# Optimization experiments

Hardware: AMD Instinct MI355X
Metric: run time of the kernel (lower is better)

## Reference

```python
import jax, jax.numpy as jnp
import numpy as np

N = 50000      # nodes
E = 1600000    # edges
IN = 128       # in_dim
HID = 128      # hidden_dim
H = 8          # heads
C = HID // H   # out_channels per head
ED = 32        # edge_feat_dim
EPS = 1e-5


def layer_norm(x, g, b):
    mu = x.mean(-1, keepdims=True)
    var = ((x - mu) ** 2).mean(-1, keepdims=True)
    return (x - mu) * jax.lax.rsqrt(var + EPS) * g + b


def setup_inputs() -> dict:
    key = jax.random.key(0)
    ks = jax.random.split(key, 24)
    w = lambda k, s, sc=0.05: (jax.random.normal(k, s, jnp.float32) * sc)
    return dict(
        x=jax.random.normal(ks[0], (N, IN), jnp.float32),
        edge_index=jax.random.randint(ks[1], (2, E), 0, N),
        edge_feats=jax.random.normal(ks[2], (E, ED), jnp.float32),
        # TransformerConv params
        Wq=w(ks[3], (IN, HID)), bq=jnp.zeros((HID,), jnp.float32),
        Wk=w(ks[4], (IN, HID)), bk=jnp.zeros((HID,), jnp.float32),
        Wv=w(ks[5], (IN, HID)), bv=jnp.zeros((HID,), jnp.float32),
        We=w(ks[6], (ED, HID)), be=jnp.zeros((HID,), jnp.float32),
        Wskip=w(ks[7], (IN, HID)), bskip=jnp.zeros((HID,), jnp.float32),
        Wbeta=w(ks[8], (3 * HID, 1)),
        ln1_g=jnp.ones((HID,), jnp.float32), ln1_b=jnp.zeros((HID,), jnp.float32),
        # GlobalContextLayer params
        Wr=w(ks[9], (HID, HID)), br=jnp.zeros((HID,), jnp.float32),
        Ww=w(ks[10], (HID, HID)), bw=jnp.zeros((HID,), jnp.float32),
        Wg=w(ks[11], (2 * HID, HID)), bg=jnp.zeros((HID,), jnp.float32),
        ln2_g=jnp.ones((HID,), jnp.float32), ln2_b=jnp.zeros((HID,), jnp.float32),
    )


def reference(x, edge_index, edge_feats,
              Wq, bq, Wk, bk, Wv, bv, We, be, Wskip, bskip, Wbeta,
              ln1_g, ln1_b, Wr, br, Ww, bw, Wg, bg, ln2_g, ln2_b):
    src, dst = edge_index[0], edge_index[1]  # messages flow src -> dst
    q = (x @ Wq + bq).reshape(N, H, C)
    k = (x @ Wk + bk).reshape(N, H, C)
    v = (x @ Wv + bv).reshape(N, H, C)
    e = (edge_feats @ We + be).reshape(E, H, C)

    k_e = k[src] + e                                   # [E,H,C]
    alpha = (q[dst] * k_e).sum(-1) / jnp.sqrt(jnp.float32(C))  # [E,H]
    # segment softmax over incoming edges of each dst node
    m = jax.ops.segment_max(alpha, dst, num_segments=N)        # [N,H]
    ex = jnp.exp(alpha - m[dst])
    s = jax.ops.segment_sum(ex, dst, num_segments=N)
    alpha = ex / (s[dst] + 1e-16)                      # [E,H]

    msg = (v[src] + e) * alpha[..., None]              # [E,H,C]
    out = jax.ops.segment_sum(msg, dst, num_segments=N).reshape(N, HID)

    # beta skip connection
    x_r = x @ Wskip + bskip
    beta = jax.nn.sigmoid(jnp.concatenate([out, x_r, out - x_r], -1) @ Wbeta)  # [N,1]
    out = beta * x_r + (1.0 - beta) * out

    # block: relu(LN(dropout(out) + residual)); dropout=0, residual_proj=None
    h = jax.nn.relu(layer_norm(out + x, ln1_g, ln1_b))

    # GlobalContextLayer
    g = jax.nn.relu(h.mean(0) @ Wr + br)               # [HID]
    g_bc = g @ Ww + bw                                 # [HID], broadcast to all nodes
    gate = jax.nn.sigmoid(jnp.concatenate([h, jnp.broadcast_to(g_bc, h.shape)], -1) @ Wg + bg)
    return layer_norm(h + gate * g_bc, ln2_g, ln2_b)
```

## Files before the change

kernel.cpp:

```cpp
#include <hip/hip_runtime.h>
#include <hip/hip_fp16.h>

#define NN 50000
#define EE 1600000
#define NB_HIST 1024
#define NB_PROJ 1563
#define NB_SCAN 49

typedef float f4v __attribute__((ext_vector_type(4)));

static __device__ __forceinline__ float4 f4z() { return make_float4(0.f, 0.f, 0.f, 0.f); }


__global__ __launch_bounds__(1024) void scan1_kernel(const int* __restrict__ counts,
                                                     int* __restrict__ offsets,
                                                     int* __restrict__ bsum)
{
    __shared__ int wsum[16];
    __shared__ int wpre[16];
    const int t = threadIdx.x;
    const int lane = t & 63, wid = t >> 6;
    const int i = blockIdx.x * 1024 + t;
    int orig = (i < NN) ? counts[i] : 0;
    int val = orig;
    #pragma unroll
    for (int ofs = 1; ofs < 64; ofs <<= 1) {
        int n = __shfl_up(val, ofs);
        if (lane >= ofs) val += n;
    }
    if (lane == 63) wsum[wid] = val;
    __syncthreads();
    if (t < 16) {
        int w = wsum[t];
        #pragma unroll
        for (int ofs = 1; ofs < 16; ofs <<= 1) {
            int n = __shfl_up(w, ofs);
            if (t >= ofs) w += n;
        }
        wpre[t] = w;
    }
    __syncthreads();
    int incl = val + (wid ? wpre[wid - 1] : 0);
    if (i < NN) offsets[i] = incl - orig;
    if (t == 1023) bsum[blockIdx.x] = incl;
}

__global__ __launch_bounds__(64) void scan2_kernel(int* __restrict__ bsum,
                                                   int* __restrict__ bpre)
{
    const int t = threadIdx.x;
    int orig = (t < NB_SCAN) ? bsum[t] : 0;
    int val = orig;
    #pragma unroll
    for (int ofs = 1; ofs < 64; ofs <<= 1) {
        int n = __shfl_up(val, ofs);
        if (t >= ofs) val += n;
    }
    if (t < NB_SCAN) bpre[t] = val - orig;
}

__global__ __launch_bounds__(1024) void scan3_kernel(int* __restrict__ offsets,
                                                     int* __restrict__ cursor,
                                                     const int* __restrict__ bpre)
{
    const int i = blockIdx.x * 1024 + threadIdx.x;
    const int add = bpre[blockIdx.x];
    if (i < NN) {
        int off = offsets[i] + add;
        offsets[i] = off;
        cursor[i] = off;
    } else if (i == NN) {
        offsets[NN] = EE;
    }
}


__global__ __launch_bounds__(256) void scatter_kernel(const int* __restrict__ ei,
                                                      int* __restrict__ cursor,
                                                      int2* __restrict__ sorted2)
{
    int i = blockIdx.x * blockDim.x + threadIdx.x;
    int stride = gridDim.x * blockDim.x;
    for (; i < EE; i += stride) {
        int srcn = ei[i];
        int d = ei[EE + i];
        int pos = atomicAdd(&cursor[d], 1);
        sorted2[pos] = make_int2(i, srcn);
    }
    if (blockIdx.x == 0 && threadIdx.x < 32) sorted2[EE + threadIdx.x] = make_int2(0, 0);
}


__global__ __launch_bounds__(256) void k1_kernel(
    const int* __restrict__ ei, int* __restrict__ counts,
    const float* __restrict__ x,
    const float* __restrict__ Wq, const float* __restrict__ bq,
    const float* __restrict__ Wk, const float* __restrict__ bk,
    const float* __restrict__ Wv, const float* __restrict__ bv,
    const float* __restrict__ Ws, const float* __restrict__ bs,
    const float* __restrict__ We,
    float* __restrict__ q, __half2* __restrict__ kvh,
    float* __restrict__ xr, __half* __restrict__ qeh)
{
    const int tid = threadIdx.x;
    if (blockIdx.x < NB_HIST) {
        int i = blockIdx.x * 256 + tid;
        int stride = NB_HIST * 256;
        for (; i < EE; i += stride) atomicAdd(&counts[ei[EE + i]], 1);
        return;
    }
    __shared__ float xs[32][132];
    __shared__ float WeS[32 * 129];
    const int row0 = (blockIdx.x - NB_HIST) * 32;
    for (int i = tid; i < 4096; i += 256) WeS[(i >> 7) * 129 + (i & 127)] = We[i];
    for (int i = tid; i < 1024; i += 256) {
        int r = i >> 5, c4 = i & 31;
        int gr = row0 + r;
        float4 val = f4z();
        if (gr < NN) val = ((const float4*)(x + (size_t)gr * 128))[c4];
        ((float4*)xs[r])[c4] = val;
    }
    __syncthreads();
    const int cg = tid & 31;
    const int rg = tid >> 5;
    float4 aq[4], ak[4], av[4], as_[4];
    #pragma unroll
    for (int r = 0; r < 4; ++r) { aq[r] = f4z(); ak[r] = f4z(); av[r] = f4z(); as_[r] = f4z(); }
    #pragma unroll 2
    for (int kk = 0; kk < 128; ++kk) {
        float4 wq = ((const float4*)(Wq + kk * 128))[cg];
        float4 wk = ((const float4*)(Wk + kk * 128))[cg];
        float4 wv = ((const float4*)(Wv + kk * 128))[cg];
        float4 ws = ((const float4*)(Ws + kk * 128))[cg];
        #pragma unroll
        for (int r = 0; r < 4; ++r) {
            float xv = xs[4 * rg + r][kk];
            aq[r].x += xv * wq.x; aq[r].y += xv * wq.y; aq[r].z += xv * wq.z; aq[r].w += xv * wq.w;
            ak[r].x += xv * wk.x; ak[r].y += xv * wk.y; ak[r].z += xv * wk.z; ak[r].w += xv * wk.w;
            av[r].x += xv * wv.x; av[r].y += xv * wv.y; av[r].z += xv * wv.z; av[r].w += xv * wv.w;
            as_[r].x += xv * ws.x; as_[r].y += xv * ws.y; as_[r].z += xv * ws.z; as_[r].w += xv * ws.w;
        }
    }
    const float4 bq4 = ((const float4*)bq)[cg];
    const float4 bk4 = ((const float4*)bk)[cg];
    const float4 bv4 = ((const float4*)bv)[cg];
    const float4 bs4 = ((const float4*)bs)[cg];
    __syncthreads();
    #pragma unroll
    for (int r = 0; r < 4; ++r) {
        int gr = row0 + 4 * rg + r;
        if (gr >= NN) continue;
        float4 o;
        o.x = aq[r].x + bq4.x; o.y = aq[r].y + bq4.y; o.z = aq[r].z + bq4.z; o.w = aq[r].w + bq4.w;
        ((float4*)(q + (size_t)gr * 128))[cg] = o;
        ((float4*)xs[4 * rg + r])[cg] = o;
        float kx = ak[r].x + bk4.x, ky = ak[r].y + bk4.y, kz = ak[r].z + bk4.z, kw = ak[r].w + bk4.w;
        float vx = av[r].x + bv4.x, vy = av[r].y + bv4.y, vz = av[r].z + bv4.z, vw = av[r].w + bv4.w;
        union { __half2 h2[4]; float4 f4; } up;
        up.h2[0] = __floats2half2_rn(kx, vx);
        up.h2[1] = __floats2half2_rn(ky, vy);
        up.h2[2] = __floats2half2_rn(kz, vz);
        up.h2[3] = __floats2half2_rn(kw, vw);
        *((float4*)(kvh + (size_t)gr * 128 + 4 * cg)) = up.f4;
        o.x = as_[r].x + bs4.x; o.y = as_[r].y + bs4.y; o.z = as_[r].z + bs4.z; o.w = as_[r].w + bs4.w;
        ((float4*)(xr + (size_t)gr * 128))[cg] = o;
    }
    __syncthreads();
    const int row = tid >> 3;
    const int j = tid & 7;
    const int gr2 = row0 + row;
    if (gr2 < NN) {
        const float* xrow = xs[row];
        #pragma unroll
        for (int hh = 0; hh < 8; ++hh) {
            float a0 = 0.f, a1 = 0.f, a2 = 0.f, a3 = 0.f;
            #pragma unroll
            for (int c = 0; c < 16; ++c) {
                float qv = xrow[hh * 16 + c];
                const float* wb = &WeS[(j * 4) * 129 + hh * 16 + c];
                a0 += qv * wb[0];
                a1 += qv * wb[129];
                a2 += qv * wb[258];
                a3 += qv * wb[387];
            }
            union { __half2 h2[2]; unsigned long long u64; } u;
            u.h2[0] = __floats2half2_rn(a0, a1);
            u.h2[1] = __floats2half2_rn(a2, a3);
            *(unsigned long long*)(qeh + (size_t)gr2 * 256 + hh * 32 + j * 4) = u.u64;
        }
    }
}


__global__ __launch_bounds__(256) void attn_kernel(
    const float* __restrict__ efeat,
    const float* __restrict__ We, const float* __restrict__ be,
    const float* __restrict__ q, const __half* __restrict__ qeh,
    const __half2* __restrict__ kvh,
    const float* __restrict__ xr, const float* __restrict__ x,
    const float* __restrict__ Wbeta,
    const float* __restrict__ ln1g, const float* __restrict__ ln1b,
    const int* __restrict__ offsets, const int2* __restrict__ sorted2,
    float* __restrict__ h, float* __restrict__ colsum)
{
    __shared__ float WeS[32][128];
    __shared__ float cs[4][128];
    const int tid = threadIdx.x;
    for (int i = tid; i < 4096; i += 256) ((float*)WeS)[i] = We[i];
    const int lane = tid & 63;
    const int wid = tid >> 6;
    const int f0 = 2 * lane;
    const int l8 = lane & 7;
    const int grp = lane & 56;

    const float be0 = be[f0], be1 = be[f0 + 1];
    const float wbo0 = Wbeta[f0],       wbo1 = Wbeta[f0 + 1];
    const float wbr0 = Wbeta[128 + f0], wbr1 = Wbeta[128 + f0 + 1];
    const float wbd0 = Wbeta[256 + f0], wbd1 = Wbeta[256 + f0 + 1];
    const float lg0 = ln1g[f0], lg1 = ln1g[f0 + 1];
    const float lb0 = ln1b[f0], lb1 = ln1b[f0 + 1];

    cs[wid][f0] = 0.f; cs[wid][f0 + 1] = 0.f;
    __syncthreads();

    const int gwave = blockIdx.x * 4 + wid;
    const int nwave = gridDim.x * 4;

    for (int node = gwave; node < NN; node += nwave) {
        const int beg = offsets[node];
        const int end = offsets[node + 1];
        const float2 qv = *(const float2*)(q + (size_t)node * 128 + f0);
        union { float2 f2; __half2 h2[2]; } uq;
        uq.f2 = *(const float2*)(qeh + (size_t)node * 256 + 4 * lane);
        const float2 qe01 = __half22float2(uq.h2[0]);
        const float2 qe23 = __half22float2(uq.h2[1]);
        const float4 qev = make_float4(qe01.x, qe01.y, qe23.x, qe23.y);
        float qbe = qv.x * be0 + qv.y * be1;
        qbe += __shfl_xor(qbe, 1); qbe += __shfl_xor(qbe, 2); qbe += __shfl_xor(qbe, 4);
        const float qbe25 = qbe * 0.25f;

        float m = -1e30f, s = 0.f, a0 = 0.f, a1 = 0.f;
        float4 wef = f4z();

        if (beg < end) {
            int2 esA[8], esB[8];
            f4v efA[8], efB[8];
            float2 kvA[8], kvB[8];

            #pragma unroll
            for (int u = 0; u < 8; ++u) esA[u] = sorted2[beg + u];
            #pragma unroll
            for (int u = 0; u < 8; ++u) {
                efA[u] = __builtin_nontemporal_load(
                    (const f4v*)(efeat + (size_t)esA[u].x * 32 + 4 * l8));
                kvA[u] = *(const float2*)(kvh + (size_t)esA[u].y * 128 + f0);
            }
            #pragma unroll
            for (int u = 0; u < 8; ++u) esB[u] = sorted2[beg + 8 + u];

            auto phase = [&](f4v (&efC)[8], float2 (&kvC)[8],
                             f4v (&efN)[8], float2 (&kvN)[8],
                             int2 (&idxN)[8], int2 (&idxF)[8], int t) {
                #pragma unroll
                for (int u = 0; u < 8; ++u) {
                    efN[u] = __builtin_nontemporal_load(
                        (const f4v*)(efeat + (size_t)idxN[u].x * 32 + 4 * l8));
                    kvN[u] = *(const float2*)(kvh + (size_t)idxN[u].y * 128 + f0);
                }
                #pragma unroll
                for (int u = 0; u < 8; ++u) idxF[u] = sorted2[t + 16 + u];

                const int cnt = end - t;
                float lgt[8]; float2 vfl[8];
                #pragma unroll
                for (int u = 0; u < 8; ++u) {
                    union { float2 f2; __half2 h2[2]; } uk; uk.f2 = kvC[u];
                    float2 k0v0 = __half22float2(uk.h2[0]);
                    float2 k1v1 = __half22float2(uk.h2[1]);
                    vfl[u] = make_float2(k0v0.y, k1v1.y);
                    float part = qv.x * k0v0.x + qv.y * k1v1.x
                               + qev.x * efC[u][0] + qev.y * efC[u][1]
                               + qev.z * efC[u][2] + qev.w * efC[u][3];
                    part += __shfl_xor(part, 1);
                    part += __shfl_xor(part, 2);
                    part += __shfl_xor(part, 4);
                    lgt[u] = (u < cnt) ? (part * 0.25f + qbe25) : -1e30f;
                }
                float m01 = fmaxf(lgt[0], lgt[1]), m23 = fmaxf(lgt[2], lgt[3]);
                float m45 = fmaxf(lgt[4], lgt[5]), m67 = fmaxf(lgt[6], lgt[7]);
                float bm = fmaxf(fmaxf(m01, m23), fmaxf(m45, m67));
                float p[8];
                #pragma unroll
                for (int u = 0; u < 8; ++u) p[u] = __expf(lgt[u] - bm);
                float bsA = 0.f, bsB = 0.f, b0A = 0.f, b0B = 0.f, b1A = 0.f, b1B = 0.f;
                float4 befA = f4z(), befB = f4z();
                #pragma unroll
                for (int u = 0; u < 8; u += 2) {
                    bsA += p[u];     bsB += p[u + 1];
                    b0A = fmaf(p[u], vfl[u].x, b0A);        b0B = fmaf(p[u + 1], vfl[u + 1].x, b0B);
                    b1A = fmaf(p[u], vfl[u].y, b1A);        b1B = fmaf(p[u + 1], vfl[u + 1].y, b1B);
                    befA.x = fmaf(p[u], efC[u][0], befA.x); befB.x = fmaf(p[u + 1], efC[u + 1][0], befB.x);
                    befA.y = fmaf(p[u], efC[u][1], befA.y); befB.y = fmaf(p[u + 1], efC[u + 1][1], befB.y);
                    befA.z = fmaf(p[u], efC[u][2], befA.z); befB.z = fmaf(p[u + 1], efC[u + 1][2], befB.z);
                    befA.w = fmaf(p[u], efC[u][3], befA.w); befB.w = fmaf(p[u + 1], efC[u + 1][3], befB.w);
                }
                const float nm = fmaxf(m, bm);
                const float so = __expf(m - nm);
                const float sn = __expf(bm - nm);
                s  = s  * so + (bsA + bsB) * sn;
                a0 = a0 * so + (b0A + b0B) * sn;
                a1 = a1 * so + (b1A + b1B) * sn;
                wef.x = wef.x * so + (befA.x + befB.x) * sn;
                wef.y = wef.y * so + (befA.y + befB.y) * sn;
                wef.z = wef.z * so + (befA.z + befB.z) * sn;
                wef.w = wef.w * so + (befA.w + befB.w) * sn;
                m = nm;
            };

            int t = beg;
            while (true) {
                phase(efA, kvA, efB, kvB, esB, esA, t); t += 8; if (t >= end) break;
                phase(efB, kvB, efA, kvA, esA, esB, t); t += 8; if (t >= end) break;
            }
        }

        const float inv = 1.f / (s + 1e-16f);
        float o0 = fmaf(a0, inv, be0);
        float o1 = fmaf(a1, inv, be1);
        float wn0 = wef.x * inv, wn1 = wef.y * inv, wn2 = wef.z * inv, wn3 = wef.w * inv;
        float ew0 = 0.f, ew1 = 0.f;
        #pragma unroll
        for (int l2 = 0; l2 < 8; ++l2) {
            float b0 = __shfl(wn0, grp + l2);
            float b1 = __shfl(wn1, grp + l2);
            float b2 = __shfl(wn2, grp + l2);
            float b3 = __shfl(wn3, grp + l2);
            float2 w0 = *(const float2*)&WeS[4 * l2 + 0][f0];
            float2 w1 = *(const float2*)&WeS[4 * l2 + 1][f0];
            float2 w2 = *(const float2*)&WeS[4 * l2 + 2][f0];
            float2 w3 = *(const float2*)&WeS[4 * l2 + 3][f0];
            ew0 += b0 * w0.x + b1 * w1.x + b2 * w2.x + b3 * w3.x;
            ew1 += b0 * w0.y + b1 * w1.y + b2 * w2.y + b3 * w3.y;
        }
        o0 += ew0; o1 += ew1;
        if (end == beg) { o0 = 0.f; o1 = 0.f; }

        const float2 xrv = *(const float2*)(xr + (size_t)node * 128 + f0);
        float bp = o0 * wbo0 + o1 * wbo1 + xrv.x * wbr0 + xrv.y * wbr1
                 + (o0 - xrv.x) * wbd0 + (o1 - xrv.y) * wbd1;
        #pragma unroll
        for (int msk = 1; msk < 64; msk <<= 1) bp += __shfl_xor(bp, msk);
        const float beta = 1.f / (1.f + __expf(-bp));
        const float2 xv = *(const float2*)(x + (size_t)node * 128 + f0);
        float t0 = beta * xrv.x + (1.f - beta) * o0 + xv.x;
        float t1 = beta * xrv.y + (1.f - beta) * o1 + xv.y;
        float sm = t0 + t1, sq = t0 * t0 + t1 * t1;
        #pragma unroll
        for (int msk = 1; msk < 64; msk <<= 1) { sm += __shfl_xor(sm, msk); sq += __shfl_xor(sq, msk); }
        const float mu = sm * (1.f / 128.f);
        const float var = sq * (1.f / 128.f) - mu * mu;
        const float rstd = rsqrtf(var + 1e-5f);
        const float h0 = fmaxf((t0 - mu) * rstd * lg0 + lb0, 0.f);
        const float h1 = fmaxf((t1 - mu) * rstd * lg1 + lb1, 0.f);
        *(float2*)(h + (size_t)node * 128 + f0) = make_float2(h0, h1);
        cs[wid][f0] += h0; cs[wid][f0 + 1] += h1;
    }
    __syncthreads();
    if (wid == 0) {
        float c0 = cs[0][f0] + cs[1][f0] + cs[2][f0] + cs[3][f0];
        float c1 = cs[0][f0 + 1] + cs[1][f0 + 1] + cs[2][f0 + 1] + cs[3][f0 + 1];
        atomicAdd(&colsum[f0], c0);
        atomicAdd(&colsum[f0 + 1], c1);
    }
}


__global__ __launch_bounds__(1024) void gctx_kernel(
    const float* __restrict__ colsum,
    const float* __restrict__ Wr, const float* __restrict__ br,
    const float* __restrict__ Ww, const float* __restrict__ bw,
    const float* __restrict__ Wg, const float* __restrict__ bg,
    float* __restrict__ gc)
{
    __shared__ float hm[128], g[128], gb[128];
    __shared__ float red[8][128];
    const int t = threadIdx.x, f = t & 127, sl = t >> 7;
    if (sl == 0) hm[f] = colsum[f] * (1.f / (float)NN);
    __syncthreads();
    float a = 0.f;
    #pragma unroll
    for (int j = 0; j < 16; ++j) { int i = sl * 16 + j; a += hm[i] * Wr[i * 128 + f]; }
    red[sl][f] = a;
    __syncthreads();
    if (sl == 0) {
        float s = br[f];
        #pragma unroll
        for (int j = 0; j < 8; ++j) s += red[j][f];
        g[f] = fmaxf(s, 0.f);
    }
    __syncthreads();
    a = 0.f;
    #pragma unroll
    for (int j = 0; j < 16; ++j) { int i = sl * 16 + j; a += g[i] * Ww[i * 128 + f]; }
    red[sl][f] = a;
    __syncthreads();
    if (sl == 0) {
        float s = bw[f];
        #pragma unroll
        for (int j = 0; j < 8; ++j) s += red[j][f];
        gb[f] = s;
        gc[f] = s;
    }
    __syncthreads();
    a = 0.f;
    #pragma unroll
    for (int j = 0; j < 16; ++j) { int i = sl * 16 + j; a += gb[i] * Wg[(128 + i) * 128 + f]; }
    red[sl][f] = a;
    __syncthreads();
    if (sl == 0) {
        float s = bg[f];
        #pragma unroll
        for (int j = 0; j < 8; ++j) s += red[j][f];
        gc[128 + f] = s;
    }
}


__global__ __launch_bounds__(256) void final_kernel(
    const float* __restrict__ h, const float* __restrict__ Wg,
    const float* __restrict__ gc,
    const float* __restrict__ ln2g, const float* __restrict__ ln2b,
    float* __restrict__ out)
{
    __shared__ float hs[32][128];
    __shared__ float ys[32][128];
    const int tid = threadIdx.x;
    const int row0 = blockIdx.x * 32;
    for (int i = tid; i < 1024; i += 256) {
        int r = i >> 5, c4 = i & 31;
        int gr = row0 + r;
        float4 val = f4z();
        if (gr < NN) val = ((const float4*)(h + (size_t)gr * 128))[c4];
        ((float4*)hs[r])[c4] = val;
    }
    __syncthreads();
    const int cg = tid & 31;
    const int rg = tid >> 5;
    float4 a[4];
    #pragma unroll
    for (int r = 0; r < 4; ++r) a[r] = f4z();
    #pragma unroll 2
    for (int kk = 0; kk < 128; ++kk) {
        float4 w4 = ((const float4*)(Wg + kk * 128))[cg];
        #pragma unroll
        for (int r = 0; r < 4; ++r) {
            float xv = hs[4 * rg + r][kk];
            a[r].x += xv * w4.x; a[r].y += xv * w4.y; a[r].z += xv * w4.z; a[r].w += xv * w4.w;
        }
    }
    const float4 gb = ((const float4*)gc)[cg];
    const float4 c2 = ((const float4*)(gc + 128))[cg];
    #pragma unroll
    for (int r = 0; r < 4; ++r) {
        int row = 4 * rg + r;
        float4 hv = ((float4*)hs[row])[cg];
        float4 y;
        float gx;
        gx = 1.f / (1.f + __expf(-(a[r].x + c2.x))); y.x = hv.x + gx * gb.x;
        gx = 1.f / (1.f + __expf(-(a[r].y + c2.y))); y.y = hv.y + gx * gb.y;
        gx = 1.f / (1.f + __expf(-(a[r].z + c2.z))); y.z = hv.z + gx * gb.z;
        gx = 1.f / (1.f + __expf(-(a[r].w + c2.w))); y.w = hv.w + gx * gb.w;
        ((float4*)ys[row])[cg] = y;
    }
    __syncthreads();
    const int lane = tid & 63;
    const int wid = tid >> 6;
    const int f0 = 2 * lane;
    const float lg0 = ln2g[f0], lg1 = ln2g[f0 + 1];
    const float lb0 = ln2b[f0], lb1 = ln2b[f0 + 1];
    for (int rr = 0; rr < 8; ++rr) {
        int row = wid * 8 + rr;
        int gr = row0 + row;
        if (gr >= NN) continue;
        float y0 = ys[row][f0], y1 = ys[row][f0 + 1];
        float sm = y0 + y1, sq = y0 * y0 + y1 * y1;
        #pragma unroll
        for (int msk = 1; msk < 64; msk <<= 1) { sm += __shfl_xor(sm, msk); sq += __shfl_xor(sq, msk); }
        float mu = sm * (1.f / 128.f);
        float var = sq * (1.f / 128.f) - mu * mu;
        float rstd = rsqrtf(var + 1e-5f);
        float o0 = (y0 - mu) * rstd * lg0 + lb0;
        float o1 = (y1 - mu) * rstd * lg1 + lb1;
        *(float2*)(out + (size_t)gr * 128 + f0) = make_float2(o0, o1);
    }
}


extern "C" void kernel_launch(void* const* d_in, const int* in_sizes, int n_in,
                              void* d_out, int out_size, void* d_ws, size_t ws_size,
                              hipStream_t stream)
{
    const float* x    = (const float*)d_in[0];
    const int*   ei   = (const int*)d_in[1];
    const float* ef   = (const float*)d_in[2];
    const float* Wq   = (const float*)d_in[3];
    const float* bq   = (const float*)d_in[4];
    const float* Wk   = (const float*)d_in[5];
    const float* bk   = (const float*)d_in[6];
    const float* Wv   = (const float*)d_in[7];
    const float* bv   = (const float*)d_in[8];
    const float* We   = (const float*)d_in[9];
    const float* be   = (const float*)d_in[10];
    const float* Wsk  = (const float*)d_in[11];
    const float* bsk  = (const float*)d_in[12];
    const float* Wbeta= (const float*)d_in[13];
    const float* g1   = (const float*)d_in[14];
    const float* b1   = (const float*)d_in[15];
    const float* Wr   = (const float*)d_in[16];
    const float* br   = (const float*)d_in[17];
    const float* Ww   = (const float*)d_in[18];
    const float* bw   = (const float*)d_in[19];
    const float* Wg   = (const float*)d_in[20];
    const float* bg   = (const float*)d_in[21];
    const float* g2   = (const float*)d_in[22];
    const float* b2   = (const float*)d_in[23];
    float* out = (float*)d_out;

    const size_t NF = (size_t)NN * 128;
    float* q      = (float*)d_ws;
    float* xr     = q + NF;
    float* h      = xr + NF;
    __half2* kvh  = (__half2*)(h + NF);
    __half* qeh   = (__half*)(kvh + NF);
    float* colsum = (float*)(qeh + (size_t)NN * 256);
    float* gc     = colsum + 128;
    int* counts   = (int*)(gc + 256);
    int* offsets  = counts + NN;
    int* cursor   = offsets + NN + 2;
    int* bsum     = cursor + NN;
    int* bpre     = bsum + 64;
    int2* sorted2 = (int2*)(bpre + 64);

    hipMemsetAsync(counts, 0, NN * sizeof(int), stream);
    hipMemsetAsync(colsum, 0, 128 * sizeof(float), stream);

    k1_kernel<<<NB_HIST + NB_PROJ, 256, 0, stream>>>(ei, counts, x,
        Wq, bq, Wk, bk, Wv, bv, Wsk, bsk, We, q, kvh, xr, qeh);
    scan1_kernel<<<NB_SCAN, 1024, 0, stream>>>(counts, offsets, bsum);
    scan2_kernel<<<1, 64, 0, stream>>>(bsum, bpre);
    scan3_kernel<<<NB_SCAN + 1, 1024, 0, stream>>>(offsets, cursor, bpre);
    scatter_kernel<<<2048, 256, 0, stream>>>(ei, cursor, sorted2);
    attn_kernel<<<2048, 256, 0, stream>>>(ef, We, be, q, qeh, kvh, xr, x, Wbeta, g1, b1,
                                          offsets, sorted2, h, colsum);
    gctx_kernel<<<1, 1024, 0, stream>>>(colsum, Wr, br, Ww, bw, Wg, bg, gc);
    final_kernel<<<(NN + 31) / 32, 256, 0, stream>>>(h, Wg, gc, g2, b2, out);
}
```

Measured before the change: 688.5 us.

## Compute Q/K/V/skip projections with bf16 MFMA using prepacked weights

Adds a small kernel that converts Wq/Wk/Wv/Wskip to bf16 and packs them into MFMA operand layout. The projection stage of k1 then computes all four projections with 16x16x32 bf16 MFMA instead of scalar FP32 FMAs, one wave per weight matrix, staging results through shared memory. The qe computation also switches from a shared-memory copy of We to vectorised global reads. This lowers FP32 ALU cost but adds bf16 rounding of x and the weights, plus an extra launch and more LDS traffic.

```diff
diff --git a/kernel.cpp b/kernel.cpp
--- a/kernel.cpp
+++ b/kernel.cpp
@@ -8,8 +8,38 @@
 #define NB_SCAN 49
 
 typedef float f4v __attribute__((ext_vector_type(4)));
+typedef __attribute__((ext_vector_type(8))) short bf16x8;
+typedef __attribute__((ext_vector_type(4))) float f32x4;
 
 static __device__ __forceinline__ float4 f4z() { return make_float4(0.f, 0.f, 0.f, 0.f); }
+
+static __device__ __forceinline__ unsigned short f2bf(float f)
+{
+    unsigned u = __float_as_uint(f);
+    u += 0x7FFF + ((u >> 16) & 1);
+    return (unsigned short)(u >> 16);
+}
+
+
+__global__ __launch_bounds__(256) void wpack_kernel(
+    const float* __restrict__ Wq, const float* __restrict__ Wk,
+    const float* __restrict__ Wv, const float* __restrict__ Ws,
+    unsigned short* __restrict__ wp)
+{
+    int idx = blockIdx.x * 256 + threadIdx.x;
+    if (idx >= 8192) return;
+    int l = idx & 63;
+    int t = (idx >> 6) & 7;
+    int s = (idx >> 9) & 3;
+    int w = idx >> 11;
+    const float* W = (w == 0) ? Wq : (w == 1) ? Wk : (w == 2) ? Wv : Ws;
+    int n = t * 16 + (l & 15);
+    int kb = s * 32 + (l >> 4) * 8;
+    union { unsigned short u16[8]; uint4 v4; } u;
+    #pragma unroll
+    for (int j = 0; j < 8; ++j) u.u16[j] = f2bf(W[(kb + j) * 128 + n]);
+    ((uint4*)wp)[idx] = u.v4;
+}
 
 
 __global__ __launch_bounds__(1024) void scan1_kernel(const int* __restrict__ counts,
@@ -94,10 +124,9 @@
 __global__ __launch_bounds__(256) void k1_kernel(
     const int* __restrict__ ei, int* __restrict__ counts,
     const float* __restrict__ x,
-    const float* __restrict__ Wq, const float* __restrict__ bq,
-    const float* __restrict__ Wk, const float* __restrict__ bk,
-    const float* __restrict__ Wv, const float* __restrict__ bv,
-    const float* __restrict__ Ws, const float* __restrict__ bs,
+    const unsigned short* __restrict__ wp,
+    const float* __restrict__ bq, const float* __restrict__ bk,
+    const float* __restrict__ bv, const float* __restrict__ bs,
     const float* __restrict__ We,
     float* __restrict__ q, __half2* __restrict__ kvh,
     float* __restrict__ xr, __half* __restrict__ qeh)
@@ -109,79 +138,125 @@
         for (; i < EE; i += stride) atomicAdd(&counts[ei[EE + i]], 1);
         return;
     }
-    __shared__ float xs[32][132];
-    __shared__ float WeS[32 * 129];
+    __shared__ unsigned short xsb[32][136];
+    __shared__ float qs[32][132];
+    __shared__ __half ks[32][128];
+    __shared__ __half vs[32][128];
+
     const int row0 = (blockIdx.x - NB_HIST) * 32;
-    for (int i = tid; i < 4096; i += 256) WeS[(i >> 7) * 129 + (i & 127)] = We[i];
+
     for (int i = tid; i < 1024; i += 256) {
         int r = i >> 5, c4 = i & 31;
         int gr = row0 + r;
         float4 val = f4z();
         if (gr < NN) val = ((const float4*)(x + (size_t)gr * 128))[c4];
-        ((float4*)xs[r])[c4] = val;
-    }
-    __syncthreads();
-    const int cg = tid & 31;
-    const int rg = tid >> 5;
-    float4 aq[4], ak[4], av[4], as_[4];
-    #pragma unroll
-    for (int r = 0; r < 4; ++r) { aq[r] = f4z(); ak[r] = f4z(); av[r] = f4z(); as_[r] = f4z(); }
-    #pragma unroll 2
-    for (int kk = 0; kk < 128; ++kk) {
-        float4 wq = ((const float4*)(Wq + kk * 128))[cg];
-        float4 wk = ((const float4*)(Wk + kk * 128))[cg];
-        float4 wv = ((const float4*)(Wv + kk * 128))[cg];
-        float4 ws = ((const float4*)(Ws + kk * 128))[cg];
-        #pragma unroll
-        for (int r = 0; r < 4; ++r) {
-            float xv = xs[4 * rg + r][kk];
-            aq[r].x += xv * wq.x; aq[r].y += xv * wq.y; aq[r].z += xv * wq.z; aq[r].w += xv * wq.w;
-            ak[r].x += xv * wk.x; ak[r].y += xv * wk.y; ak[r].z += xv * wk.z; ak[r].w += xv * wk.w;
-            av[r].x += xv * wv.x; av[r].y += xv * wv.y; av[r].z += xv * wv.z; av[r].w += xv * wv.w;
-            as_[r].x += xv * ws.x; as_[r].y += xv * ws.y; as_[r].z += xv * ws.z; as_[r].w += xv * ws.w;
+        union { unsigned short u16[4]; uint2 v; } u;
+        u.u16[0] = f2bf(val.x); u.u16[1] = f2bf(val.y);
+        u.u16[2] = f2bf(val.z); u.u16[3] = f2bf(val.w);
+        *(uint2*)&xsb[r][c4 * 4] = u.v;
+    }
+    __syncthreads();
+
+    const int lane = tid & 63;
+    const int w = tid >> 6;
+    const int lr = (lane >> 4) * 4;
+    const int lc = lane & 15;
+
+    f32x4 acc[2][8];
+    #pragma unroll
+    for (int mt = 0; mt < 2; ++mt)
+        #pragma unroll
+        for (int t = 0; t < 8; ++t)
+            acc[mt][t] = (f32x4){0.f, 0.f, 0.f, 0.f};
+
+    const bf16x8* wp8 = (const bf16x8*)wp;
+    #pragma unroll
+    for (int s = 0; s < 4; ++s) {
+        bf16x8 a0 = *(const bf16x8*)&xsb[lc][s * 32 + (lane >> 4) * 8];
+        bf16x8 a1 = *(const bf16x8*)&xsb[16 + lc][s * 32 + (lane >> 4) * 8];
+        #pragma unroll
+        for (int t = 0; t < 8; ++t) {
+            bf16x8 b = wp8[((w * 4 + s) * 8 + t) * 64 + lane];
+            acc[0][t] = __builtin_amdgcn_mfma_f32_16x16x32_bf16(a0, b, acc[0][t], 0, 0, 0);
+            acc[1][t] = __builtin_amdgcn_mfma_f32_16x16x32_bf16(a1, b, acc[1][t], 0, 0, 0);
         }
     }
-    const float4 bq4 = ((const float4*)bq)[cg];
-    const float4 bk4 = ((const float4*)bk)[cg];
-    const float4 bv4 = ((const float4*)bv)[cg];
-    const float4 bs4 = ((const float4*)bs)[cg];
-    __syncthreads();
-    #pragma unroll
-    for (int r = 0; r < 4; ++r) {
-        int gr = row0 + 4 * rg + r;
+
+    const float* bias = (w == 0) ? bq : (w == 1) ? bk : (w == 2) ? bv : bs;
+    float bc[8];
+    #pragma unroll
+    for (int t = 0; t < 8; ++t) bc[t] = bias[t * 16 + lc];
+
+    if (w == 0) {
+        #pragma unroll
+        for (int mt = 0; mt < 2; ++mt)
+            #pragma unroll
+            for (int t = 0; t < 8; ++t)
+                #pragma unroll
+                for (int i = 0; i < 4; ++i)
+                    qs[mt * 16 + lr + i][t * 16 + lc] = acc[mt][t][i] + bc[t];
+    } else if (w == 1) {
+        #pragma unroll
+        for (int mt = 0; mt < 2; ++mt)
+            #pragma unroll
+            for (int t = 0; t < 8; ++t)
+                #pragma unroll
+                for (int i = 0; i < 4; ++i)
+                    ks[mt * 16 + lr + i][t * 16 + lc] = __float2half(acc[mt][t][i] + bc[t]);
+    } else if (w == 2) {
+        #pragma unroll
+        for (int mt = 0; mt < 2; ++mt)
+            #pragma unroll
+            for (int t = 0; t < 8; ++t)
+                #pragma unroll
+                for (int i = 0; i < 4; ++i)
+                    vs[mt * 16 + lr + i][t * 16 + lc] = __float2half(acc[mt][t][i] + bc[t]);
+    } else {
+        #pragma unroll
+        for (int mt = 0; mt < 2; ++mt)
+            #pragma unroll
+            for (int t = 0; t < 8; ++t)
+                #pragma unroll
+                for (int i = 0; i < 4; ++i) {
+                    int gr = row0 + mt * 16 + lr + i;
+                    if (gr < NN) xr[(size_t)gr * 128 + t * 16 + lc] = acc[mt][t][i] + bc[t];
+                }
+    }
+    __syncthreads();
+
+    for (int i = tid; i < 1024; i += 256) {
+        int r = i >> 5, c4 = i & 31;
+        int gr = row0 + r;
         if (gr >= NN) continue;
-        float4 o;
-        o.x = aq[r].x + bq4.x; o.y = aq[r].y + bq4.y; o.z = aq[r].z + bq4.z; o.w = aq[r].w + bq4.w;
-        ((float4*)(q + (size_t)gr * 128))[cg] = o;
-        ((float4*)xs[4 * rg + r])[cg] = o;
-        float kx = ak[r].x + bk4.x, ky = ak[r].y + bk4.y, kz = ak[r].z + bk4.z, kw = ak[r].w + bk4.w;
-        float vx = av[r].x + bv4.x, vy = av[r].y + bv4.y, vz = av[r].z + bv4.z, vw = av[r].w + bv4.w;
+        float4 qv = make_float4(qs[r][4 * c4], qs[r][4 * c4 + 1],
+                                qs[r][4 * c4 + 2], qs[r][4 * c4 + 3]);
+        ((float4*)(q + (size_t)gr * 128))[c4] = qv;
         union { __half2 h2[4]; float4 f4; } up;
-        up.h2[0] = __floats2half2_rn(kx, vx);
-        up.h2[1] = __floats2half2_rn(ky, vy);
-        up.h2[2] = __floats2half2_rn(kz, vz);
-        up.h2[3] = __floats2half2_rn(kw, vw);
-        *((float4*)(kvh + (size_t)gr * 128 + 4 * cg)) = up.f4;
-        o.x = as_[r].x + bs4.x; o.y = as_[r].y + bs4.y; o.z = as_[r].z + bs4.z; o.w = as_[r].w + bs4.w;
-        ((float4*)(xr + (size_t)gr * 128))[cg] = o;
-    }
-    __syncthreads();
+        #pragma unroll
+        for (int c = 0; c < 4; ++c)
+            up.h2[c] = __halves2half2(ks[r][4 * c4 + c], vs[r][4 * c4 + c]);
+        *((float4*)(kvh + (size_t)gr * 128 + 4 * c4)) = up.f4;
+    }
+
     const int row = tid >> 3;
     const int j = tid & 7;
     const int gr2 = row0 + row;
     if (gr2 < NN) {
-        const float* xrow = xs[row];
+        const float* xrow = qs[row];
         #pragma unroll
         for (int hh = 0; hh < 8; ++hh) {
             float a0 = 0.f, a1 = 0.f, a2 = 0.f, a3 = 0.f;
             #pragma unroll
-            for (int c = 0; c < 16; ++c) {
-                float qv = xrow[hh * 16 + c];
-                const float* wb = &WeS[(j * 4) * 129 + hh * 16 + c];
-                a0 += qv * wb[0];
-                a1 += qv * wb[129];
-                a2 += qv * wb[258];
-                a3 += qv * wb[387];
+            for (int cc = 0; cc < 4; ++cc) {
+                float4 xv = *(const float4*)&xrow[hh * 16 + 4 * cc];
+                float4 w0 = *(const float4*)&We[(j * 4 + 0) * 128 + hh * 16 + 4 * cc];
+                float4 w1 = *(const float4*)&We[(j * 4 + 1) * 128 + hh * 16 + 4 * cc];
+                float4 w2 = *(const float4*)&We[(j * 4 + 2) * 128 + hh * 16 + 4 * cc];
+                float4 w3 = *(const float4*)&We[(j * 4 + 3) * 128 + hh * 16 + 4 * cc];
+                a0 += xv.x * w0.x + xv.y * w0.y + xv.z * w0.z + xv.w * w0.w;
+                a1 += xv.x * w1.x + xv.y * w1.y + xv.z * w1.z + xv.w * w1.w;
+                a2 += xv.x * w2.x + xv.y * w2.y + xv.z * w2.z + xv.w * w2.w;
+                a3 += xv.x * w3.x + xv.y * w3.y + xv.z * w3.z + xv.w * w3.w;
             }
             union { __half2 h2[2]; unsigned long long u64; } u;
             u.h2[0] = __floats2half2_rn(a0, a1);
@@ -534,7 +609,8 @@
     __half* qeh   = (__half*)(kvh + NF);
     float* colsum = (float*)(qeh + (size_t)NN * 256);
     float* gc     = colsum + 128;
-    int* counts   = (int*)(gc + 256);
+    unsigned short* wpk = (unsigned short*)(gc + 256);
+    int* counts   = (int*)(wpk + 65536);
     int* offsets  = counts + NN;
     int* cursor   = offsets + NN + 2;
     int* bsum     = cursor + NN;
@@ -544,8 +620,9 @@
     hipMemsetAsync(counts, 0, NN * sizeof(int), stream);
     hipMemsetAsync(colsum, 0, 128 * sizeof(float), stream);
 
-    k1_kernel<<<NB_HIST + NB_PROJ, 256, 0, stream>>>(ei, counts, x,
-        Wq, bq, Wk, bk, Wv, bv, Wsk, bsk, We, q, kvh, xr, qeh);
+    wpack_kernel<<<32, 256, 0, stream>>>(Wq, Wk, Wv, Wsk, wpk);
+    k1_kernel<<<NB_HIST + NB_PROJ, 256, 0, stream>>>(ei, counts, x, wpk,
+        bq, bk, bv, bsk, We, q, kvh, xr, qeh);
     scan1_kernel<<<NB_SCAN, 1024, 0, stream>>>(counts, offsets, bsum);
     scan2_kernel<<<1, 64, 0, stream>>>(bsum, bpre);
     scan3_kernel<<<NB_SCAN + 1, 1024, 0, stream>>>(offsets, cursor, bpre);
```

After: 687.2 us. Within noise of the previous version (-0.2%).
